# Kernel optimization log

Measured on AMD Instinct MI355X. Metric: run time of the kernel, lower is better.

The kernel has to match this reference:

```python
import jax, jax.numpy as jnp
import numpy as np

N_NODES = 2048
EMBED = 256
STATE = 128
HID = 256
N_ACT = 256
TEAMS = 8
PAIR_F = 14


def setup_inputs() -> dict:
    key = jax.random.key(0)
    ks = jax.random.split(key, 12)
    B, T = 16, 32
    node_embeddings = jax.random.normal(ks[0], (N_NODES, EMBED), jnp.float32)
    states = jax.random.normal(ks[1], (B, T, STATE), jnp.float32)
    pair_features = jax.random.normal(ks[2], (B, T, N_ACT, PAIR_F), jnp.float32)
    proc_action_indices = jax.random.randint(ks[3], (N_ACT,), 0, N_NODES)
    in_dim = EMBED * 4 + PAIR_F
    s = lambda k, sh, fan: jax.random.normal(k, sh, jnp.float32) / np.sqrt(fan)
    return {
        "node_embeddings": node_embeddings,
        "states": states,
        "pair_features": pair_features,
        "proc_action_indices": proc_action_indices,
        "team_table": jax.random.normal(ks[4], (TEAMS, EMBED), jnp.float32),
        "Ws": s(ks[5], (STATE, EMBED), STATE),
        "bs": jnp.zeros((EMBED,), jnp.float32),
        "W1": s(ks[6], (in_dim, HID), in_dim),
        "b1": jnp.zeros((HID,), jnp.float32),
        "W2": s(ks[7], (HID, HID), HID),
        "b2": jnp.zeros((HID,), jnp.float32),
        "W3": s(ks[8], (HID, 1), HID),
        "b3": jnp.zeros((1,), jnp.float32),
    }


def reference(node_embeddings, states, pair_features, proc_action_indices,
              team_table, Ws, bs, W1, b1, W2, b2, W3, b3):
    B, T, A, F = pair_features.shape
    team_ids = jnp.arange(A) % TEAMS  # registered buffer
    # [A, E] gathered / per-action embeddings
    proc_emb = node_embeddings[proc_action_indices]          # [A, E]
    team_emb = team_table[team_ids]                          # [A, E]
    global_emb = jnp.mean(node_embeddings, axis=0)           # [E]
    state_emb = jax.nn.relu(states @ Ws + bs)                # [B, T, E]
    # broadcast + concat -> [B, T, A, 4E + F]
    bT = (B, T, A)
    scorer_input = jnp.concatenate([
        jnp.broadcast_to(proc_emb[None, None], bT + (proc_emb.shape[-1],)),
        jnp.broadcast_to(team_emb[None, None], bT + (team_emb.shape[-1],)),
        jnp.broadcast_to(global_emb[None, None, None], bT + (global_emb.shape[-1],)),
        jnp.broadcast_to(state_emb[:, :, None], bT + (state_emb.shape[-1],)),
        pair_features,
    ], axis=-1)
    h = jax.nn.relu(scorer_input @ W1 + b1)
    h = jax.nn.relu(h @ W2 + b2)
    scores = (h @ W3 + b3)[..., 0]  # [B, T, A]
    return scores[:, :, None, :]    # [B, T, 1, A]
```

## Files before the change

### kernel.cpp

```cpp
#include <hip/hip_runtime.h>
#include <hip/hip_bf16.h>

#define N_NODES 2048
#define EMBED 256
#define STATE 128
#define HID 256
#define N_ACT 256
#define TEAMS 8
#define PAIR_F 14
#define BT_TOTAL 512
#define M_TOTAL (BT_TOTAL * N_ACT)

typedef _Float16 f16_t;
typedef _Float16 f16x8 __attribute__((ext_vector_type(8)));
typedef _Float16 f16x4 __attribute__((ext_vector_type(4)));
typedef float f32x4 __attribute__((ext_vector_type(4)));

__device__ __forceinline__ size_t reord_idx(int k, int n, int KB) {
    return (size_t)(((n >> 4) * KB + (k >> 5)) * 4 + ((k >> 3) & 3)) * 128 +
           (size_t)(n & 15) * 8 + (k & 7);
}

__device__ __forceinline__ size_t par_idx(int a, int n) {
    return (size_t)(a >> 4) * 4096 + (size_t)(n >> 2) * 64 + (a & 15) * 4 + (n & 3);
}

__global__ void k_cs(const float* __restrict__ ne, float* __restrict__ gpart) {
    int b = blockIdx.x;
    int t = threadIdx.x;
    float s = 0.f;
    const float* base = ne + (size_t)b * 32 * EMBED + t;
#pragma unroll
    for (int i = 0; i < 32; ++i) s += base[(size_t)i * EMBED];
    gpart[b * EMBED + t] = s;
}

__global__ void k_prep(const float* __restrict__ ne, const int* __restrict__ idx,
                       const float* __restrict__ team, const float* __restrict__ states,
                       const float* __restrict__ Ws, const float* __restrict__ W1,
                       const float* __restrict__ W2, const float* __restrict__ gpart,
                       f16_t* __restrict__ vecs, f16_t* __restrict__ W1abT,
                       f16_t* __restrict__ W1cT, f16_t* __restrict__ W1dT,
                       f16_t* __restrict__ WsT, f16_t* __restrict__ W2s,
                       f16_t* __restrict__ w1pt, f16_t* __restrict__ states_h,
                       f16_t* __restrict__ gm_h) {
    int i = blockIdx.x * 256 + threadIdx.x;
    if (i < 131072) {
        int a = i >> 9, e = i & 511;
        float v = (e < 256) ? ne[(size_t)idx[a] * EMBED + e]
                            : team[(a % TEAMS) * EMBED + (e - 256)];
        vecs[i] = (f16_t)v;
        return;
    }
    i -= 131072;
    if (i < 131072) {
        int k = i >> 8, n = i & 255;
        W1abT[reord_idx(k, n, 16)] = (f16_t)W1[(size_t)k * HID + n];
        return;
    }
    i -= 131072;
    if (i < 65536) {
        int k = i >> 8, n = i & 255;
        W1cT[reord_idx(k, n, 8)] = (f16_t)W1[(size_t)(512 + k) * HID + n];
        return;
    }
    i -= 65536;
    if (i < 65536) {
        int k = i >> 8, n = i & 255;
        W1dT[reord_idx(k, n, 8)] = (f16_t)W1[(size_t)(768 + k) * HID + n];
        return;
    }
    i -= 65536;
    if (i < 32768) {
        int k = i >> 8, n = i & 255;
        WsT[reord_idx(k, n, 4)] = (f16_t)Ws[(size_t)k * EMBED + n];
        return;
    }
    i -= 32768;
    if (i < 65536) {
        int k = i >> 8, n = i & 255;
        W2s[reord_idx(k, n, 8)] = (f16_t)W2[(size_t)k * HID + n];
        return;
    }
    i -= 65536;
    if (i < 8192) {
        int k = i >> 8, n = i & 255;
        float v = (k < PAIR_F) ? W1[(size_t)(1024 + k) * HID + n] : 0.f;
        w1pt[reord_idx(k, n, 1)] = (f16_t)v;
        return;
    }
    i -= 8192;
    if (i < 65536) { states_h[i] = (f16_t)states[i]; return; }
    i -= 65536;
    if (i < 256) {
        float s = 0.f;
#pragma unroll 8
        for (int p = 0; p < 64; ++p) s += gpart[p * EMBED + i];
        gm_h[i] = (f16_t)(s * (1.0f / N_NODES));
    }
}

__global__ __launch_bounds__(256, 4) void k_pp(
    const f16_t* __restrict__ states_h, const f16_t* __restrict__ WsT,
    const float* __restrict__ bs, const f16_t* __restrict__ W1dT,
    const f16_t* __restrict__ vecs, const f16_t* __restrict__ W1abT,
    const f16_t* __restrict__ W1cT, const f16_t* __restrict__ gm_h,
    const float* __restrict__ b1, f16_t* __restrict__ paR,
    f16_t* __restrict__ pbt_h) {
    __shared__ __align__(16) f16_t se[64 * 256];
    const int tid = threadIdx.x;
    const int wid = tid >> 6, lane = tid & 63;
    const int c = lane & 15, q = lane >> 4;
    int bid = blockIdx.x;

    if (bid >= 8) {
        int b = bid - 8;
        const int m0 = (b >> 2) * 64, n0 = (b & 3) * 64;
        const int n = n0 + wid * 16 + c;
        const int g = n >> 4;
        f32x4 acc[4] = {f32x4{0,0,0,0}, f32x4{0,0,0,0}, f32x4{0,0,0,0}, f32x4{0,0,0,0}};
        for (int ks = 0; ks < 16; ++ks) {
            f16x8 bf = *(const f16x8*)(W1abT + (size_t)((g * 16 + ks) * 4 + q) * 128 + c * 8);
#pragma unroll
            for (int mi = 0; mi < 4; ++mi) {
                f16x8 af = *(const f16x8*)(vecs + (size_t)(m0 + mi * 16 + c) * 512 + ks * 32 + q * 8);
                acc[mi] = __builtin_amdgcn_mfma_f32_16x16x32_f16(af, bf, acc[mi], 0, 0, 0);
            }
        }
#pragma unroll
        for (int ks = 0; ks < 8; ++ks) {
            f16x8 bf = *(const f16x8*)(W1cT + (size_t)((g * 8 + ks) * 4 + q) * 128 + c * 8);
            f16x8 af = *(const f16x8*)(gm_h + ks * 32 + q * 8);
#pragma unroll
            for (int mi = 0; mi < 4; ++mi)
                acc[mi] = __builtin_amdgcn_mfma_f32_16x16x32_f16(af, bf, acc[mi], 0, 0, 0);
        }
        float b1v = b1[n];
#pragma unroll
        for (int mi = 0; mi < 4; ++mi)
#pragma unroll
            for (int j = 0; j < 4; ++j) {
                int a = m0 + mi * 16 + q * 4 + j;
                paR[par_idx(a, n)] = (f16_t)(acc[mi][j] + b1v);
            }
        return;
    }

    const int bt0 = bid * 64;
    f32x4 acc[4][4];
#pragma unroll
    for (int mi = 0; mi < 4; ++mi)
#pragma unroll
        for (int ni = 0; ni < 4; ++ni) acc[mi][ni] = f32x4{0, 0, 0, 0};
#pragma unroll
    for (int ks = 0; ks < 4; ++ks) {
        f16x8 bh[4];
#pragma unroll
        for (int ni = 0; ni < 4; ++ni) {
            int g = wid * 4 + ni;
            bh[ni] = *(const f16x8*)(WsT + (size_t)((g * 4 + ks) * 4 + q) * 128 + c * 8);
        }
#pragma unroll
        for (int mi = 0; mi < 4; ++mi) {
            f16x8 af = *(const f16x8*)(states_h + (size_t)(bt0 + mi * 16 + c) * STATE + ks * 32 + q * 8);
#pragma unroll
            for (int ni = 0; ni < 4; ++ni)
                acc[mi][ni] = __builtin_amdgcn_mfma_f32_16x16x32_f16(af, bh[ni], acc[mi][ni], 0, 0, 0);
        }
    }
#pragma unroll
    for (int mi = 0; mi < 4; ++mi)
#pragma unroll
        for (int ni = 0; ni < 4; ++ni) {
            float bsv = bs[wid * 64 + ni * 16 + c];
#pragma unroll
            for (int j = 0; j < 4; ++j) {
                int m = mi * 16 + q * 4 + j;
                int n = wid * 64 + ni * 16 + c;
                se[m * 256 + (n ^ ((m & 7) << 3))] = (f16_t)fmaxf(acc[mi][ni][j] + bsv, 0.f);
            }
        }
#pragma unroll
    for (int mi = 0; mi < 4; ++mi)
#pragma unroll
        for (int ni = 0; ni < 4; ++ni) acc[mi][ni] = f32x4{0, 0, 0, 0};
    __syncthreads();
#pragma unroll
    for (int ks = 0; ks < 8; ++ks) {
        f16x8 bh[4];
#pragma unroll
        for (int ni = 0; ni < 4; ++ni) {
            int g = wid * 4 + ni;
            bh[ni] = *(const f16x8*)(W1dT + (size_t)((g * 8 + ks) * 4 + q) * 128 + c * 8);
        }
#pragma unroll
        for (int mi = 0; mi < 4; ++mi) {
            int m = mi * 16 + c;
            f16x8 ah = *(const f16x8*)(&se[m * 256 + ((ks * 32 + q * 8) ^ ((m & 7) << 3))]);
#pragma unroll
            for (int ni = 0; ni < 4; ++ni)
                acc[mi][ni] = __builtin_amdgcn_mfma_f32_16x16x32_f16(ah, bh[ni], acc[mi][ni], 0, 0, 0);
        }
    }
#pragma unroll
    for (int mi = 0; mi < 4; ++mi)
#pragma unroll
        for (int ni = 0; ni < 4; ++ni)
#pragma unroll
            for (int j = 0; j < 4; ++j)
                pbt_h[(size_t)(bt0 + mi * 16 + q * 4 + j) * HID + wid * 64 + ni * 16 + c] =
                    (f16_t)acc[mi][ni][j];
}

__global__ __launch_bounds__(256, 4) void k_main(
    const float* __restrict__ pf, const f16_t* __restrict__ paR,
    const f16_t* __restrict__ pbt, const f16_t* __restrict__ w2s,
    const f16_t* __restrict__ w1pt, const float* __restrict__ b2,
    const float* __restrict__ W3, const float* __restrict__ b3,
    float* __restrict__ out) {
    __shared__ __align__(16) f16_t Ah[64 * 256];
    __shared__ __align__(16) float pfs[64 * PAIR_F];
    __shared__ float red[4][64];

    const int tid = threadIdx.x;
    const int wc = tid >> 6, lane = tid & 63;
    const int c = lane & 15, q = lane >> 4;

    const int r0 = blockIdx.x * 64;
    const int bt = r0 >> 8;
    const int a0 = r0 & 255;

    if (tid < 224) {
        const float4 v = ((const float4*)(pf + (size_t)r0 * PAIR_F))[tid];
        *(float4*)&pfs[tid * 4] = v;
    }

    f32x4 acc[16];
#pragma unroll
    for (int i = 0; i < 16; ++i) acc[i] = f32x4{0, 0, 0, 0};

    f16x8 af[4];
#pragma unroll
    for (int nf = 0; nf < 4; ++nf) {
        int g = wc * 4 + nf;
        af[nf] = *(const f16x8*)(w1pt + (size_t)(g * 4 + q) * 128 + c * 8);
    }

    __syncthreads();

#pragma unroll
    for (int mf = 0; mf < 4; ++mf) {
        int m = mf * 16 + c;
        f16x8 bf;
#pragma unroll
        for (int j = 0; j < 8; ++j) {
            int k = q * 8 + j;
            float v = (q < 2 && k < PAIR_F) ? pfs[m * PAIR_F + k] : 0.f;
            bf[j] = (f16_t)v;
        }
#pragma unroll
        for (int nf = 0; nf < 4; ++nf)
            acc[nf * 4 + mf] = __builtin_amdgcn_mfma_f32_16x16x32_f16(af[nf], bf, acc[nf * 4 + mf], 0, 0, 0);
    }

#pragma unroll
    for (int nf = 0; nf < 4; ++nf) {
        int n0 = wc * 64 + nf * 16 + q * 4;
        f16x4 pbtv = *(const f16x4*)(pbt + (size_t)bt * HID + n0);
#pragma unroll
        for (int mf = 0; mf < 4; ++mf) {
            int m = mf * 16 + c;
            f16x4 pav = *(const f16x4*)(paR + (size_t)((a0 >> 4) + mf) * 4096 +
                                        (size_t)(n0 >> 2) * 64 + c * 4);
            f16x4 hv;
#pragma unroll
            for (int j = 0; j < 4; ++j) {
                float h = acc[nf * 4 + mf][j] + (float)pav[j] + (float)pbtv[j];
                hv[j] = (f16_t)fmaxf(h, 0.f);
            }
            *(f16x4*)(&Ah[m * 256 + (n0 ^ ((m & 7) << 3))]) = hv;
        }
    }

#pragma unroll
    for (int i = 0; i < 16; ++i) acc[i] = f32x4{0, 0, 0, 0};

    __syncthreads();

    f16x8 bh[4];
#pragma unroll
    for (int ni = 0; ni < 4; ++ni) {
        int g = wc * 4 + ni;
        bh[ni] = *(const f16x8*)(w2s + (size_t)((g * 8 + 0) * 4 + q) * 128 + c * 8);
    }
#pragma unroll
    for (int ks = 0; ks < 8; ++ks) {
        f16x8 bhn[4];
        if (ks < 7) {
#pragma unroll
            for (int ni = 0; ni < 4; ++ni) {
                int g = wc * 4 + ni;
                bhn[ni] = *(const f16x8*)(w2s + (size_t)((g * 8 + ks + 1) * 4 + q) * 128 + c * 8);
            }
        }
#pragma unroll
        for (int mi = 0; mi < 4; ++mi) {
            int m = mi * 16 + c;
            int kx = (ks * 32 + q * 8) ^ ((m & 7) << 3);
            f16x8 ah = *(const f16x8*)(&Ah[m * 256 + kx]);
#pragma unroll
            for (int ni = 0; ni < 4; ++ni)
                acc[mi * 4 + ni] = __builtin_amdgcn_mfma_f32_16x16x32_f16(ah, bh[ni], acc[mi * 4 + ni], 0, 0, 0);
        }
#pragma unroll
        for (int ni = 0; ni < 4; ++ni) bh[ni] = bhn[ni];
    }

    float p[4][4];
#pragma unroll
    for (int mi = 0; mi < 4; ++mi)
#pragma unroll
        for (int j = 0; j < 4; ++j) p[mi][j] = 0.f;
#pragma unroll
    for (int ni = 0; ni < 4; ++ni) {
        int n = wc * 64 + ni * 16 + c;
        float b2v = b2[n];
        float w3v = W3[n];
#pragma unroll
        for (int mi = 0; mi < 4; ++mi)
#pragma unroll
            for (int j = 0; j < 4; ++j)
                p[mi][j] = fmaf(fmaxf(acc[mi * 4 + ni][j] + b2v, 0.f), w3v, p[mi][j]);
    }
#pragma unroll
    for (int off = 1; off < 16; off <<= 1)
#pragma unroll
        for (int mi = 0; mi < 4; ++mi)
#pragma unroll
            for (int j = 0; j < 4; ++j) p[mi][j] += __shfl_xor(p[mi][j], off, 64);

    if (c == 0) {
#pragma unroll
        for (int mi = 0; mi < 4; ++mi)
#pragma unroll
            for (int j = 0; j < 4; ++j) red[wc][mi * 16 + q * 4 + j] = p[mi][j];
    }
    __syncthreads();

    if (tid < 64) {
        out[(size_t)r0 + tid] = red[0][tid] + red[1][tid] + red[2][tid] + red[3][tid] + b3[0];
    }
}

extern "C" void kernel_launch(void* const* d_in, const int* in_sizes, int n_in,
                              void* d_out, int out_size, void* d_ws, size_t ws_size,
                              hipStream_t stream) {
    (void)in_sizes; (void)n_in; (void)out_size; (void)ws_size;
    const float* ne     = (const float*)d_in[0];
    const float* states = (const float*)d_in[1];
    const float* pf     = (const float*)d_in[2];
    const int*   idx    = (const int*)d_in[3];
    const float* team   = (const float*)d_in[4];
    const float* Ws     = (const float*)d_in[5];
    const float* bs     = (const float*)d_in[6];
    const float* W1     = (const float*)d_in[7];
    const float* b1     = (const float*)d_in[8];
    const float* W2     = (const float*)d_in[9];
    const float* b2     = (const float*)d_in[10];
    const float* W3     = (const float*)d_in[11];
    const float* b3     = (const float*)d_in[12];
    float* out = (float*)d_out;

    char* ws = (char*)d_ws;
    float* gpart    = (float*)(ws + 0);
    f16_t* vecs     = (f16_t*)(ws + 65536);
    f16_t* W1abT    = (f16_t*)(ws + 327680);
    f16_t* W1cT     = (f16_t*)(ws + 589824);
    f16_t* W1dT     = (f16_t*)(ws + 720896);
    f16_t* WsT      = (f16_t*)(ws + 851968);
    f16_t* W2s      = (f16_t*)(ws + 917504);
    f16_t* w1pt     = (f16_t*)(ws + 1048576);
    f16_t* states_h = (f16_t*)(ws + 1064960);
    f16_t* gm_h     = (f16_t*)(ws + 1196032);
    f16_t* paR      = (f16_t*)(ws + 1196544);
    f16_t* pbt_h    = (f16_t*)(ws + 1327616);

    k_cs<<<64, 256, 0, stream>>>(ne, gpart);
    k_prep<<<2209, 256, 0, stream>>>(ne, idx, team, states, Ws, W1, W2, gpart,
                                     vecs, W1abT, W1cT, W1dT, WsT, W2s, w1pt,
                                     states_h, gm_h);
    k_pp<<<24, 256, 0, stream>>>(states_h, WsT, bs, W1dT, vecs, W1abT, W1cT,
                                 gm_h, b1, paR, pbt_h);
    k_main<<<M_TOTAL / 64, 256, 0, stream>>>(pf, paR, pbt_h, W2s, w1pt, b2, W3, b3, out);
}
```

Measured before the change: 51.85 us.

## Merge column-sum into prep kernel, vectorize prep writes, finish mean in k_pp

The separate column-sum kernel becomes the first 64 blocks of the prep kernel, which removes one launch. The final reduction of the node-embedding mean moves into the k_pp blocks that consume it, with the result kept in shared memory instead of a global gm_h buffer. Prep threads now each produce 8 fp16 values and write them as one vector store, computing source indices from the reordered output index, so the grid shrinks from 2209 to 340 blocks. In exchange, every k_pp projection block repeats the 64-way reduction, and the strided gathers from the weight matrices are now serialized within each thread.

Result: faster. 49.69 us (-4.2%).

```diff
diff --git a/kernel.cpp b/kernel.cpp
--- a/kernel.cpp
+++ b/kernel.cpp
@@ -25,78 +25,97 @@
     return (size_t)(a >> 4) * 4096 + (size_t)(n >> 2) * 64 + (a & 15) * 4 + (n & 3);
 }
 
-__global__ void k_cs(const float* __restrict__ ne, float* __restrict__ gpart) {
-    int b = blockIdx.x;
-    int t = threadIdx.x;
-    float s = 0.f;
-    const float* base = ne + (size_t)b * 32 * EMBED + t;
-#pragma unroll
-    for (int i = 0; i < 32; ++i) s += base[(size_t)i * EMBED];
-    gpart[b * EMBED + t] = s;
+__device__ __forceinline__ f16x8 gather8(const float* __restrict__ W, int k0, int n, int ld) {
+    f16x8 r;
+#pragma unroll
+    for (int j = 0; j < 8; ++j) r[j] = (f16_t)W[(size_t)(k0 + j) * ld + n];
+    return r;
 }
 
 __global__ void k_prep(const float* __restrict__ ne, const int* __restrict__ idx,
                        const float* __restrict__ team, const float* __restrict__ states,
                        const float* __restrict__ Ws, const float* __restrict__ W1,
-                       const float* __restrict__ W2, const float* __restrict__ gpart,
+                       const float* __restrict__ W2, float* __restrict__ gpart,
                        f16_t* __restrict__ vecs, f16_t* __restrict__ W1abT,
                        f16_t* __restrict__ W1cT, f16_t* __restrict__ W1dT,
                        f16_t* __restrict__ WsT, f16_t* __restrict__ W2s,
-                       f16_t* __restrict__ w1pt, f16_t* __restrict__ states_h,
-                       f16_t* __restrict__ gm_h) {
-    int i = blockIdx.x * 256 + threadIdx.x;
-    if (i < 131072) {
-        int a = i >> 9, e = i & 511;
-        float v = (e < 256) ? ne[(size_t)idx[a] * EMBED + e]
-                            : team[(a % TEAMS) * EMBED + (e - 256)];
-        vecs[i] = (f16_t)v;
-        return;
-    }
-    i -= 131072;
-    if (i < 131072) {
-        int k = i >> 8, n = i & 255;
-        W1abT[reord_idx(k, n, 16)] = (f16_t)W1[(size_t)k * HID + n];
-        return;
-    }
-    i -= 131072;
-    if (i < 65536) {
-        int k = i >> 8, n = i & 255;
-        W1cT[reord_idx(k, n, 8)] = (f16_t)W1[(size_t)(512 + k) * HID + n];
-        return;
-    }
-    i -= 65536;
-    if (i < 65536) {
-        int k = i >> 8, n = i & 255;
-        W1dT[reord_idx(k, n, 8)] = (f16_t)W1[(size_t)(768 + k) * HID + n];
-        return;
-    }
-    i -= 65536;
-    if (i < 32768) {
-        int k = i >> 8, n = i & 255;
-        WsT[reord_idx(k, n, 4)] = (f16_t)Ws[(size_t)k * EMBED + n];
-        return;
-    }
-    i -= 32768;
-    if (i < 65536) {
-        int k = i >> 8, n = i & 255;
-        W2s[reord_idx(k, n, 8)] = (f16_t)W2[(size_t)k * HID + n];
-        return;
-    }
-    i -= 65536;
-    if (i < 8192) {
-        int k = i >> 8, n = i & 255;
-        float v = (k < PAIR_F) ? W1[(size_t)(1024 + k) * HID + n] : 0.f;
-        w1pt[reord_idx(k, n, 1)] = (f16_t)v;
-        return;
-    }
-    i -= 8192;
-    if (i < 65536) { states_h[i] = (f16_t)states[i]; return; }
-    i -= 65536;
-    if (i < 256) {
+                       f16_t* __restrict__ w1pt, f16_t* __restrict__ states_h) {
+    int bid = blockIdx.x;
+    if (bid < 64) {
+        int t = threadIdx.x;
         float s = 0.f;
-#pragma unroll 8
-        for (int p = 0; p < 64; ++p) s += gpart[p * EMBED + i];
-        gm_h[i] = (f16_t)(s * (1.0f / N_NODES));
+        const float* base = ne + (size_t)bid * 32 * EMBED + t;
+#pragma unroll
+        for (int i = 0; i < 32; ++i) s += base[(size_t)i * EMBED];
+        gpart[bid * EMBED + t] = s;
+        return;
+    }
+    int u = (bid - 64) * 256 + threadIdx.x;
+    if (u < 16384) {
+        int a = u >> 6, e = (u & 63) * 8;
+        f16x8 r;
+        if (e < 256) {
+            const float* src = ne + (size_t)idx[a] * EMBED + e;
+#pragma unroll
+            for (int j = 0; j < 8; ++j) r[j] = (f16_t)src[j];
+        } else {
+            const float* src = team + (size_t)(a % TEAMS) * EMBED + (e - 256);
+#pragma unroll
+            for (int j = 0; j < 8; ++j) r[j] = (f16_t)src[j];
+        }
+        *(f16x8*)(vecs + (size_t)u * 8) = r;
+        return;
+    }
+    u -= 16384;
+    if (u < 16384) {
+        int c = u & 15, q = (u >> 4) & 3, kb = (u >> 6) & 15, g = u >> 10;
+        *(f16x8*)(W1abT + (size_t)u * 8) = gather8(W1, kb * 32 + q * 8, g * 16 + c, HID);
+        return;
+    }
+    u -= 16384;
+    if (u < 8192) {
+        int c = u & 15, q = (u >> 4) & 3, kb = (u >> 6) & 7, g = u >> 9;
+        *(f16x8*)(W1cT + (size_t)u * 8) = gather8(W1, 512 + kb * 32 + q * 8, g * 16 + c, HID);
+        return;
+    }
+    u -= 8192;
+    if (u < 8192) {
+        int c = u & 15, q = (u >> 4) & 3, kb = (u >> 6) & 7, g = u >> 9;
+        *(f16x8*)(W1dT + (size_t)u * 8) = gather8(W1, 768 + kb * 32 + q * 8, g * 16 + c, HID);
+        return;
+    }
+    u -= 8192;
+    if (u < 4096) {
+        int c = u & 15, q = (u >> 4) & 3, kb = (u >> 6) & 3, g = u >> 8;
+        *(f16x8*)(WsT + (size_t)u * 8) = gather8(Ws, kb * 32 + q * 8, g * 16 + c, EMBED);
+        return;
+    }
+    u -= 4096;
+    if (u < 8192) {
+        int c = u & 15, q = (u >> 4) & 3, kb = (u >> 6) & 7, g = u >> 9;
+        *(f16x8*)(W2s + (size_t)u * 8) = gather8(W2, kb * 32 + q * 8, g * 16 + c, HID);
+        return;
+    }
+    u -= 8192;
+    if (u < 1024) {
+        int c = u & 15, q = (u >> 4) & 3, g = u >> 6;
+        int n = g * 16 + c, k0 = q * 8;
+        f16x8 r;
+#pragma unroll
+        for (int j = 0; j < 8; ++j) {
+            int k = k0 + j;
+            r[j] = (f16_t)((k < PAIR_F) ? W1[(size_t)(1024 + k) * HID + n] : 0.f);
+        }
+        *(f16x8*)(w1pt + (size_t)u * 8) = r;
+        return;
+    }
+    u -= 1024;
+    if (u < 8192) {
+        const float* src = states + (size_t)u * 8;
+        f16x8 r;
+#pragma unroll
+        for (int j = 0; j < 8; ++j) r[j] = (f16_t)src[j];
+        *(f16x8*)(states_h + (size_t)u * 8) = r;
     }
 }
 
@@ -104,16 +123,24 @@
     const f16_t* __restrict__ states_h, const f16_t* __restrict__ WsT,
     const float* __restrict__ bs, const f16_t* __restrict__ W1dT,
     const f16_t* __restrict__ vecs, const f16_t* __restrict__ W1abT,
-    const f16_t* __restrict__ W1cT, const f16_t* __restrict__ gm_h,
+    const f16_t* __restrict__ W1cT, const float* __restrict__ gpart,
     const float* __restrict__ b1, f16_t* __restrict__ paR,
     f16_t* __restrict__ pbt_h) {
     __shared__ __align__(16) f16_t se[64 * 256];
+    __shared__ __align__(16) f16_t gml[256];
     const int tid = threadIdx.x;
     const int wid = tid >> 6, lane = tid & 63;
     const int c = lane & 15, q = lane >> 4;
     int bid = blockIdx.x;
 
     if (bid >= 8) {
+        {
+            float s = 0.f;
+#pragma unroll 8
+            for (int p = 0; p < 64; ++p) s += gpart[p * EMBED + tid];
+            gml[tid] = (f16_t)(s * (1.0f / N_NODES));
+        }
+        __syncthreads();
         int b = bid - 8;
         const int m0 = (b >> 2) * 64, n0 = (b & 3) * 64;
         const int n = n0 + wid * 16 + c;
@@ -130,7 +157,7 @@
 #pragma unroll
         for (int ks = 0; ks < 8; ++ks) {
             f16x8 bf = *(const f16x8*)(W1cT + (size_t)((g * 8 + ks) * 4 + q) * 128 + c * 8);
-            f16x8 af = *(const f16x8*)(gm_h + ks * 32 + q * 8);
+            f16x8 af = *(const f16x8*)(gml + ks * 32 + q * 8);
 #pragma unroll
             for (int mi = 0; mi < 4; ++mi)
                 acc[mi] = __builtin_amdgcn_mfma_f32_16x16x32_f16(af, bf, acc[mi], 0, 0, 0);
@@ -381,15 +408,13 @@
     f16_t* W2s      = (f16_t*)(ws + 917504);
     f16_t* w1pt     = (f16_t*)(ws + 1048576);
     f16_t* states_h = (f16_t*)(ws + 1064960);
-    f16_t* gm_h     = (f16_t*)(ws + 1196032);
-    f16_t* paR      = (f16_t*)(ws + 1196544);
-    f16_t* pbt_h    = (f16_t*)(ws + 1327616);
-
-    k_cs<<<64, 256, 0, stream>>>(ne, gpart);
-    k_prep<<<2209, 256, 0, stream>>>(ne, idx, team, states, Ws, W1, W2, gpart,
-                                     vecs, W1abT, W1cT, W1dT, WsT, W2s, w1pt,
-                                     states_h, gm_h);
+    f16_t* paR      = (f16_t*)(ws + 1196032);
+    f16_t* pbt_h    = (f16_t*)(ws + 1327104);
+
+    k_prep<<<64 + 276, 256, 0, stream>>>(ne, idx, team, states, Ws, W1, W2, gpart,
+                                         vecs, W1abT, W1cT, W1dT, WsT, W2s, w1pt,
+                                         states_h);
     k_pp<<<24, 256, 0, stream>>>(states_h, WsT, bs, W1dT, vecs, W1abT, W1cT,
-                                 gm_h, b1, paR, pbt_h);
+                                 gpart, b1, paR, pbt_h);
     k_main<<<M_TOTAL / 64, 256, 0, stream>>>(pf, paR, pbt_h, W2s, w1pt, b2, W3, b3, out);
 }
```
